# Performance work log

Hardware: AMD Instinct MI355X
Metric: run time of the kernel (lower is better)

## Reference

```python
import jax, jax.numpy as jnp
import numpy as np

VOCAB, EMBED, HIDDEN, NCLS = 50257, 64, 64, 5
B, S = 4096, 512
BN_EPS = 1e-5


def setup_inputs() -> dict:
    key = jax.random.key(0)
    ks = jax.random.split(key, 10)
    x = jax.random.randint(ks[0], (B, S), 0, VOCAB, dtype=jnp.int64 if jax.config.jax_enable_x64 else jnp.int32)
    emb = jax.random.normal(ks[1], (VOCAB, EMBED), dtype=jnp.float32)
    emb = emb.at[0].set(0.0)  # padding_idx=0
    s = 1.0 / np.sqrt(HIDDEN)
    W_ih = jax.random.uniform(ks[2], (HIDDEN, EMBED), minval=-s, maxval=s, dtype=jnp.float32)
    W_hh = jax.random.uniform(ks[3], (HIDDEN, HIDDEN), minval=-s, maxval=s, dtype=jnp.float32)
    b_ih = jax.random.uniform(ks[4], (HIDDEN,), minval=-s, maxval=s, dtype=jnp.float32)
    b_hh = jax.random.uniform(ks[5], (HIDDEN,), minval=-s, maxval=s, dtype=jnp.float32)
    gamma = jnp.ones((HIDDEN,), dtype=jnp.float32)
    beta = jnp.zeros((HIDDEN,), dtype=jnp.float32)
    sf = 1.0 / np.sqrt(HIDDEN)
    W_fc = jax.random.uniform(ks[6], (NCLS, HIDDEN), minval=-sf, maxval=sf, dtype=jnp.float32)
    b_fc = jax.random.uniform(ks[7], (NCLS,), minval=-sf, maxval=sf, dtype=jnp.float32)
    return {"x": x, "emb": emb, "W_ih": W_ih, "W_hh": W_hh, "b_ih": b_ih,
            "b_hh": b_hh, "gamma": gamma, "beta": beta, "W_fc": W_fc, "b_fc": b_fc}


def reference(x, emb, W_ih, W_hh, b_ih, b_hh, gamma, beta, W_fc, b_fc):
    # embedding gather: [B, S, E]
    xe = emb[x]
    # precompute input projection once: [B, S, H] -> scan over time as [S, B, H]
    xp = jnp.einsum('bse,he->bsh', xe, W_ih) + b_ih + b_hh
    xp_t = jnp.swapaxes(xp, 0, 1)

    def step(h, xt):
        h = jnp.tanh(xt + h @ W_hh.T)
        return h, None

    h0 = jnp.zeros((x.shape[0], HIDDEN), dtype=xp.dtype)
    h_n, _ = jax.lax.scan(step, h0, xp_t)

    # BatchNorm1d (training-mode math: batch stats, biased variance)
    mean = jnp.mean(h_n, axis=0)
    var = jnp.mean((h_n - mean) ** 2, axis=0)
    h_bn = (h_n - mean) * jax.lax.rsqrt(var + BN_EPS) * gamma + beta
    # dropout is identity in eval / deterministic reference
    logits = h_bn @ W_fc.T + b_fc  # [B, 5]
    return logits
```

## Files before the change

kernel.cpp:

```cpp
#include <hip/hip_runtime.h>

typedef unsigned short u16;
typedef __attribute__((ext_vector_type(8))) short bf16x8;
typedef __attribute__((ext_vector_type(4))) float f32x4;
typedef __attribute__((ext_vector_type(4))) u16 u16x4;

constexpr int BATCH  = 4096;
constexpr int SEQ    = 512;
constexpr int HID    = 64;
constexpr int EMB_N4 = 50257 * 64 / 4;

__device__ __forceinline__ float bf2f(u16 u) {
  union { unsigned int i; float f; } c; c.i = ((unsigned int)u) << 16; return c.f;
}
__device__ __forceinline__ u16 f2bf(float f) {
  union { float f; unsigned int i; } c; c.f = f;
  unsigned int u = c.i;
  u += 0x7fffu + ((u >> 16) & 1u);
  return (u16)(u >> 16);
}

#define MFMA16(a, b, c) __builtin_amdgcn_mfma_f32_16x16x32_bf16(a, b, c, 0, 0, 0)

__global__ __launch_bounds__(256) void prep_kernel(
    const float4* __restrict__ emb4, const float* __restrict__ Wih,
    const float* __restrict__ Whh, u16x4* __restrict__ emb_bf4,
    u16* __restrict__ wih_hi, u16* __restrict__ whh_hi, u16* __restrict__ whh_lo,
    float* __restrict__ bn_acc)
{
  int gid = blockIdx.x * 256 + threadIdx.x;
  if (gid < EMB_N4) {
    float4 v = emb4[gid];
    u16x4 o;
    o.x = f2bf(v.x); o.y = f2bf(v.y); o.z = f2bf(v.z); o.w = f2bf(v.w);
    emb_bf4[gid] = o;
  } else if (gid < EMB_N4 + 1024) {
    int i0 = (gid - EMB_N4) * 4;
    #pragma unroll
    for (int k = 0; k < 4; ++k) {
      int i = i0 + k;
      wih_hi[i] = f2bf(Wih[i]);
      float w = Whh[i];
      u16 hi = f2bf(w);
      whh_hi[i] = hi;
      whh_lo[i] = f2bf(w - bf2f(hi));
    }
  } else if (gid < EMB_N4 + 1024 + 128) {
    bn_acc[gid - (EMB_N4 + 1024)] = 0.f;
  }
}

__global__ __launch_bounds__(256, 1) void rnn_scan_kernel(
    const int* __restrict__ xx, const u16* __restrict__ emb_bf,
    const u16* __restrict__ wih_hi, const u16* __restrict__ whh_hi,
    const u16* __restrict__ whh_lo,
    const float* __restrict__ b_ih, const float* __restrict__ b_hh,
    float* __restrict__ hT , float* __restrict__ bn_acc)
{
  __shared__ u16 hbuf[2 * 2048];
  const int tid = threadIdx.x;
  const int w = tid >> 6;
  const int L = tid & 63;
  const int n = L & 15;
  const int q = L >> 4;
  const int R0 = blockIdx.x << 4;
  const int row  = R0 + n;
  const int feat = (w << 4) + n;

  ((int4*)hbuf)[tid] = int4{0, 0, 0, 0};

  bf16x8 Bih0 = *(const bf16x8*)(wih_hi + feat * 64 +      8 * q);
  bf16x8 Bih1 = *(const bf16x8*)(wih_hi + feat * 64 + 32 + 8 * q);
  bf16x8 Bh0  = *(const bf16x8*)(whh_hi + feat * 64 +      8 * q);
  bf16x8 Bh1  = *(const bf16x8*)(whh_hi + feat * 64 + 32 + 8 * q);
  bf16x8 Bl0  = *(const bf16x8*)(whh_lo + feat * 64 +      8 * q);
  bf16x8 Bl1  = *(const bf16x8*)(whh_lo + feat * 64 + 32 + 8 * q);
  const float bias = b_ih[feat] + b_hh[feat];

  const int r0off = n * 64 + (((0 + q) ^ (n & 7)) << 3);
  const int r1off = n * 64 + (((4 + q) ^ (n & 7)) << 3);
  const int cwbase = (w << 1) + (n >> 3);

  const int4* x4 = (const int4*)(xx + row * SEQ);
  int4 K1 = x4[1];

  bf16x8 e0[4], e1[4];
  {
    int4 K0 = x4[0];
    const int id0[4] = {K0.x, K0.y, K0.z, K0.w};
    #pragma unroll
    for (int u = 0; u < 4; ++u) {
      const u16* eb = emb_bf + (long)id0[u] * 64 + 8 * q;
      e0[u] = *(const bf16x8*)(eb);
      e1[u] = *(const bf16x8*)(eb + 32);
    }
  }

  __syncthreads();

  for (int t = 0; t < SEQ / 4; ++t) {
    int4 K2 = x4[(t + 2 < SEQ / 4) ? t + 2 : SEQ / 4 - 1];
    const int nid[4] = {K1.x, K1.y, K1.z, K1.w};
    const bool lastt = (t == SEQ / 4 - 1);

    #pragma unroll
    for (int u = 0; u < 4; ++u) {
      const int p = u & 1;
      const u16* hb = hbuf + p * 2048;
      bf16x8 ah0 = *(const bf16x8*)(hb + r0off);
      bf16x8 ah1 = *(const bf16x8*)(hb + r1off);
      bf16x8 al0 = *(const bf16x8*)(hb + 1024 + r0off);
      bf16x8 al1 = *(const bf16x8*)(hb + 1024 + r1off);

      f32x4 C1 = {bias, bias, bias, bias};
      C1 = MFMA16(e0[u], Bih0, C1);
      C1 = MFMA16(e1[u], Bih1, C1);

      {
        const u16* eb = emb_bf + (long)nid[u] * 64 + 8 * q;
        e0[u] = *(const bf16x8*)(eb);
        e1[u] = *(const bf16x8*)(eb + 32);
      }

      f32x4 Cx = {0.f, 0.f, 0.f, 0.f};
      f32x4 Cy = {0.f, 0.f, 0.f, 0.f};
      f32x4 Cz = {0.f, 0.f, 0.f, 0.f};
      Cx = MFMA16(ah0, Bh0, Cx);  Cx = MFMA16(al0, Bh0, Cx);
      Cy = MFMA16(ah1, Bh1, Cy);  Cy = MFMA16(al1, Bh1, Cy);
      Cz = MFMA16(ah0, Bl0, Cz);  Cz = MFMA16(ah1, Bl1, Cz);

      u16* wb = hbuf + (p ^ 1) * 2048;
      float th4[4];
      #pragma unroll
      for (int r = 0; r < 4; ++r) {
        float v = (C1[r] + Cx[r]) + (Cy[r] + Cz[r]);
        float ex = __builtin_amdgcn_exp2f(2.8853900817779268f * v);
        float th = fmaf(-2.0f, __builtin_amdgcn_rcpf(ex + 1.0f), 1.0f);
        th4[r] = th;
        const int mw = (q << 2) + r;
        const int off = mw * 64 + ((cwbase ^ (mw & 7)) << 3) + (n & 7);
        unsigned int tb = __float_as_uint(th);
        wb[off] = (u16)(tb >> 16);
        wb[1024 + off] = (u16)(__float_as_uint(th - __uint_as_float(tb & 0xffff0000u)) >> 16);
      }

      if (u == 3 && lastt) {
        float s1 = 0.f, s2 = 0.f;
        #pragma unroll
        for (int r = 0; r < 4; ++r) {
          hT[feat * BATCH + R0 + (q << 2) + r] = th4[r];
          s1 += th4[r];
          s2 = fmaf(th4[r], th4[r], s2);
        }
        s1 += __shfl_xor(s1, 16, 64);  s2 += __shfl_xor(s2, 16, 64);
        s1 += __shfl_xor(s1, 32, 64);  s2 += __shfl_xor(s2, 32, 64);
        if (q == 0) {
          atomicAdd(bn_acc + feat, s1);
          atomicAdd(bn_acc + 64 + feat, s2);
        }
      }

      asm volatile("s_waitcnt lgkmcnt(0)\n\ts_barrier" ::: "memory");
    }
    K1 = K2;
  }
}

__global__ __launch_bounds__(256) void head_kernel(
    const float* __restrict__ hT, const float* __restrict__ bn_acc,
    const float* __restrict__ gamma, const float* __restrict__ beta,
    const float* __restrict__ Wfc, const float* __restrict__ bfc,
    float* __restrict__ out)
{
  __shared__ float sc[64], sh[64];
  const int tid = threadIdx.x;
  if (tid < 64) {
    float mean = bn_acc[tid] * (1.0f / BATCH);
    float var  = bn_acc[64 + tid] * (1.0f / BATCH) - mean * mean;
    float inv  = rsqrtf(var + 1e-5f);
    float s    = gamma[tid] * inv;
    sc[tid] = s;
    sh[tid] = beta[tid] - mean * s;
  }
  __syncthreads();
  const int b = blockIdx.x * 256 + tid;
  float acc[5];
  #pragma unroll
  for (int c = 0; c < 5; ++c) acc[c] = bfc[c];
  for (int j = 0; j < HID; ++j) {
    float hv  = hT[j * BATCH + b];
    float hat = fmaf(hv, sc[j], sh[j]);
    #pragma unroll
    for (int c = 0; c < 5; ++c) acc[c] = fmaf(hat, Wfc[c * 64 + j], acc[c]);
  }
  #pragma unroll
  for (int c = 0; c < 5; ++c) out[b * 5 + c] = acc[c];
}

extern "C" void kernel_launch(void* const* d_in, const int* in_sizes, int n_in,
                              void* d_out, int out_size, void* d_ws, size_t ws_size,
                              hipStream_t stream)
{
  const int*   x     = (const int*)d_in[0];
  const float* emb   = (const float*)d_in[1];
  const float* W_ih  = (const float*)d_in[2];
  const float* W_hh  = (const float*)d_in[3];
  const float* b_ih  = (const float*)d_in[4];
  const float* b_hh  = (const float*)d_in[5];
  const float* gamma = (const float*)d_in[6];
  const float* beta  = (const float*)d_in[7];
  const float* W_fc  = (const float*)d_in[8];
  const float* b_fc  = (const float*)d_in[9];

  char* ws = (char*)d_ws;
  float* hT     = (float*)ws;
  float* bn_acc = (float*)(ws + 1048576);
  u16*   emb_bf = (u16*)(ws + 1049088);
  u16*   wih_hi = (u16*)(ws + 7481984);
  u16*   whh_hi = (u16*)(ws + 7490176);
  u16*   whh_lo = (u16*)(ws + 7498368);

  const int prep_items = EMB_N4 + 1024 + 128;
  prep_kernel<<<dim3((prep_items + 255) / 256), dim3(256), 0, stream>>>(
      (const float4*)emb, W_ih, W_hh, (u16x4*)emb_bf, wih_hi, whh_hi, whh_lo, bn_acc);
  rnn_scan_kernel<<<dim3(BATCH / 16), dim3(256), 0, stream>>>(
      x, emb_bf, wih_hi, whh_hi, whh_lo, b_ih, b_hh, hT, bn_acc);
  head_kernel<<<dim3(BATCH / 256), dim3(256), 0, stream>>>(
      hT, bn_acc, gamma, beta, W_fc, b_fc, (float*)d_out);
}
```

Baseline: 250.7 us.

## Stream embedding rows into an LDS ring via global_load_lds, pack hidden hi/lo

Instead of every wave loading embedding rows into registers, wave 0 issues asynchronous global-to-LDS DMA loads into an 8-slot shared ring several timesteps ahead, and all waves read the current slot from LDS. The hidden-state hi/lo bf16 halves are packed into one 32-bit word per element with a new swizzle, so each step needs one LDS store per value and the reads are unpacked with perm instructions. The intent is to hide embedding-gather latency and cut LDS store traffic on the serial recurrence. The cost is more LDS use, a vmcnt-based wait that only wave 0 performs, and index bookkeeping that is easy to get wrong.

Measured after the change: 315.1 us. 25.7% more time.

```diff
diff --git a/kernel.cpp b/kernel.cpp
--- a/kernel.cpp
+++ b/kernel.cpp
@@ -1,6 +1,7 @@
 #include <hip/hip_runtime.h>
 
 typedef unsigned short u16;
+typedef unsigned int u32;
 typedef __attribute__((ext_vector_type(8))) short bf16x8;
 typedef __attribute__((ext_vector_type(4))) float f32x4;
 typedef __attribute__((ext_vector_type(4))) u16 u16x4;
@@ -11,16 +12,35 @@
 constexpr int EMB_N4 = 50257 * 64 / 4;
 
 __device__ __forceinline__ float bf2f(u16 u) {
-  union { unsigned int i; float f; } c; c.i = ((unsigned int)u) << 16; return c.f;
+  union { u32 i; float f; } c; c.i = ((u32)u) << 16; return c.f;
 }
 __device__ __forceinline__ u16 f2bf(float f) {
-  union { float f; unsigned int i; } c; c.f = f;
-  unsigned int u = c.i;
+  union { float f; u32 i; } c; c.f = f;
+  u32 u = c.i;
   u += 0x7fffu + ((u >> 16) & 1u);
   return (u16)(u >> 16);
 }
 
 #define MFMA16(a, b, c) __builtin_amdgcn_mfma_f32_16x16x32_bf16(a, b, c, 0, 0, 0)
+
+__device__ __forceinline__ void glds16(const u16* g, u16* l) {
+  __builtin_amdgcn_global_load_lds(
+      (const __attribute__((address_space(1))) u32*)g,
+      (__attribute__((address_space(3))) u32*)l, 16, 0, 0);
+}
+
+__device__ __forceinline__ void unpack2(uint4 a, uint4 b, bf16x8& hi, bf16x8& lo) {
+  union { u32 u[4]; bf16x8 v; } H, L;
+  H.u[0] = __builtin_amdgcn_perm(a.y, a.x, 0x05040100u);
+  H.u[1] = __builtin_amdgcn_perm(a.w, a.z, 0x05040100u);
+  H.u[2] = __builtin_amdgcn_perm(b.y, b.x, 0x05040100u);
+  H.u[3] = __builtin_amdgcn_perm(b.w, b.z, 0x05040100u);
+  L.u[0] = __builtin_amdgcn_perm(a.y, a.x, 0x07060302u);
+  L.u[1] = __builtin_amdgcn_perm(a.w, a.z, 0x07060302u);
+  L.u[2] = __builtin_amdgcn_perm(b.y, b.x, 0x07060302u);
+  L.u[3] = __builtin_amdgcn_perm(b.w, b.z, 0x07060302u);
+  hi = H.v; lo = L.v;
+}
 
 __global__ __launch_bounds__(256) void prep_kernel(
     const float4* __restrict__ emb4, const float* __restrict__ Wih,
@@ -57,17 +77,17 @@
     const float* __restrict__ b_ih, const float* __restrict__ b_hh,
     float* __restrict__ hT , float* __restrict__ bn_acc)
 {
-  __shared__ u16 hbuf[2 * 2048];
+  __shared__ u32 hpk[2 * 1024];
+  __shared__ u16 ring[8 * 1024];
   const int tid = threadIdx.x;
   const int w = tid >> 6;
   const int L = tid & 63;
   const int n = L & 15;
   const int q = L >> 4;
   const int R0 = blockIdx.x << 4;
-  const int row  = R0 + n;
   const int feat = (w << 4) + n;
 
-  ((int4*)hbuf)[tid] = int4{0, 0, 0, 0};
+  ((int4*)hpk)[tid] = int4{0, 0, 0, 0};
 
   bf16x8 Bih0 = *(const bf16x8*)(wih_hi + feat * 64 +      8 * q);
   bf16x8 Bih1 = *(const bf16x8*)(wih_hi + feat * 64 + 32 + 8 * q);
@@ -77,50 +97,57 @@
   bf16x8 Bl1  = *(const bf16x8*)(whh_lo + feat * 64 + 32 + 8 * q);
   const float bias = b_ih[feat] + b_hh[feat];
 
-  const int r0off = n * 64 + (((0 + q) ^ (n & 7)) << 3);
-  const int r1off = n * 64 + (((4 + q) ^ (n & 7)) << 3);
-  const int cwbase = (w << 1) + (n >> 3);
-
-  const int4* x4 = (const int4*)(xx + row * SEQ);
-  int4 K1 = x4[1];
-
-  bf16x8 e0[4], e1[4];
-  {
+  const int sw   = ((n >> 2) & 1) << 4;
+  const int roff = n * 64 + ((8 * q) ^ sw);
+  const int wcol = feat ^ ((q & 1) << 4);
+  const int e0off = (q * 16 + n) * 8;
+
+  const int4* x4 = (const int4*)(xx + (R0 + n) * SEQ);
+  int4 JA = {0,0,0,0}, JB = {0,0,0,0};
+
+  if (w == 0) {
     int4 K0 = x4[0];
-    const int id0[4] = {K0.x, K0.y, K0.z, K0.w};
+    int4 K1 = x4[1];
+    const int pre[8] = {K0.x, K0.y, K0.z, K0.w, K1.x, K1.y, K1.z, 0};
+    #pragma unroll
+    for (int p = 0; p < 7; ++p) {
+      const u16* gp = emb_bf + (long)pre[p] * 64 + q * 8;
+      u16* lp = ring + p * 1024;
+      glds16(gp, lp);
+      glds16(gp + 32, lp + 512);
+    }
+    JA = K1;
+    JB = x4[2];
+  }
+
+  __syncthreads();
+
+  for (int t = 0; t < SEQ / 4; ++t) {
+    const int sbase = (t & 1) << 2;
+    int4 JC = {0,0,0,0};
+
     #pragma unroll
     for (int u = 0; u < 4; ++u) {
-      const u16* eb = emb_bf + (long)id0[u] * 64 + 8 * q;
-      e0[u] = *(const bf16x8*)(eb);
-      e1[u] = *(const bf16x8*)(eb + 32);
-    }
-  }
-
-  __syncthreads();
-
-  for (int t = 0; t < SEQ / 4; ++t) {
-    int4 K2 = x4[(t + 2 < SEQ / 4) ? t + 2 : SEQ / 4 - 1];
-    const int nid[4] = {K1.x, K1.y, K1.z, K1.w};
-    const bool lastt = (t == SEQ / 4 - 1);
-
-    #pragma unroll
-    for (int u = 0; u < 4; ++u) {
-      const int p = u & 1;
-      const u16* hb = hbuf + p * 2048;
-      bf16x8 ah0 = *(const bf16x8*)(hb + r0off);
-      bf16x8 ah1 = *(const bf16x8*)(hb + r1off);
-      bf16x8 al0 = *(const bf16x8*)(hb + 1024 + r0off);
-      bf16x8 al1 = *(const bf16x8*)(hb + 1024 + r1off);
+      const int cur = u & 1;
+      const int slot_rd  = sbase + u;
+      const int slot_dma = (sbase + u + 7) & 7;
+
+      const u16* rp = ring + slot_rd * 1024;
+      bf16x8 ae0 = *(const bf16x8*)(rp + e0off);
+      bf16x8 ae1 = *(const bf16x8*)(rp + 512 + e0off);
+
+      const u32* hb = hpk + cur * 1024;
+      uint4 vl0 = *(const uint4*)(hb + roff);
+      uint4 vl1 = *(const uint4*)(hb + roff + 4);
+      uint4 vh0 = *(const uint4*)(hb + roff + 32);
+      uint4 vh1 = *(const uint4*)(hb + roff + 36);
+      bf16x8 ah0, al0, ah1, al1;
+      unpack2(vl0, vl1, ah0, al0);
+      unpack2(vh0, vh1, ah1, al1);
 
       f32x4 C1 = {bias, bias, bias, bias};
-      C1 = MFMA16(e0[u], Bih0, C1);
-      C1 = MFMA16(e1[u], Bih1, C1);
-
-      {
-        const u16* eb = emb_bf + (long)nid[u] * 64 + 8 * q;
-        e0[u] = *(const bf16x8*)(eb);
-        e1[u] = *(const bf16x8*)(eb + 32);
-      }
+      C1 = MFMA16(ae0, Bih0, C1);
+      C1 = MFMA16(ae1, Bih1, C1);
 
       f32x4 Cx = {0.f, 0.f, 0.f, 0.f};
       f32x4 Cy = {0.f, 0.f, 0.f, 0.f};
@@ -129,7 +156,19 @@
       Cy = MFMA16(ah1, Bh1, Cy);  Cy = MFMA16(al1, Bh1, Cy);
       Cz = MFMA16(ah0, Bl0, Cz);  Cz = MFMA16(ah1, Bl1, Cz);
 
-      u16* wb = hbuf + (p ^ 1) * 2048;
+      if (w == 0) {
+        const int idxv = (u == 0) ? JA.w : (u == 1) ? JB.x : (u == 2) ? JB.y : JB.z;
+        const u16* gp = emb_bf + (long)idxv * 64 + q * 8;
+        u16* lp = ring + slot_dma * 1024;
+        glds16(gp, lp);
+        glds16(gp + 32, lp + 512);
+        if (u == 0) {
+          int tc = (t + 3 < SEQ / 4) ? t + 3 : SEQ / 4 - 1;
+          JC = x4[tc];
+        }
+      }
+
+      u32* wb = hpk + (cur ^ 1) * 1024;
       float th4[4];
       #pragma unroll
       for (int r = 0; r < 4; ++r) {
@@ -137,14 +176,13 @@
         float ex = __builtin_amdgcn_exp2f(2.8853900817779268f * v);
         float th = fmaf(-2.0f, __builtin_amdgcn_rcpf(ex + 1.0f), 1.0f);
         th4[r] = th;
-        const int mw = (q << 2) + r;
-        const int off = mw * 64 + ((cwbase ^ (mw & 7)) << 3) + (n & 7);
-        unsigned int tb = __float_as_uint(th);
-        wb[off] = (u16)(tb >> 16);
-        wb[1024 + off] = (u16)(__float_as_uint(th - __uint_as_float(tb & 0xffff0000u)) >> 16);
+        u32 tb = __float_as_uint(th);
+        u32 remb = __float_as_uint(th - __uint_as_float(tb & 0xffff0000u));
+        u32 packed = __builtin_amdgcn_perm(remb, tb, 0x07060302u);
+        wb[((q << 2) + r) * 64 + wcol] = packed;
       }
 
-      if (u == 3 && lastt) {
+      if (t == SEQ / 4 - 1 && u == 3) {
         float s1 = 0.f, s2 = 0.f;
         #pragma unroll
         for (int r = 0; r < 4; ++r) {
@@ -160,9 +198,12 @@
         }
       }
 
-      asm volatile("s_waitcnt lgkmcnt(0)\n\ts_barrier" ::: "memory");
+      if (w == 0)
+        asm volatile("s_waitcnt vmcnt(12) lgkmcnt(0)\n\ts_barrier" ::: "memory");
+      else
+        asm volatile("s_waitcnt lgkmcnt(0)\n\ts_barrier" ::: "memory");
     }
-    K1 = K2;
+    if (w == 0) { JA = JB; JB = JC; }
   }
 }
 
```

## Halve rows per RNN block to run two blocks per CU

Applied to the files above, without the earlier changes.

Each scan block now handles 8 batch rows instead of 16, so the grid doubles to 512 blocks. The launch bounds now allow two blocks per CU, which lets two independent recurrences interleave and hide MFMA, LDS and barrier latency in the serial time loop. The 16-row MFMA tile still runs in full, with the rows duplicated, so only half of the lanes write hidden state and contribute to the BN statistics. The cost is doubled MFMA work per useful row and higher register pressure, since the kernel must now fit two blocks per CU.

New measurement: 350.0 us. 39.6% more time.

```diff
diff --git a/kernel.cpp b/kernel.cpp
--- a/kernel.cpp
+++ b/kernel.cpp
@@ -1,6 +1,7 @@
 #include <hip/hip_runtime.h>
 
 typedef unsigned short u16;
+typedef unsigned int u32;
 typedef __attribute__((ext_vector_type(8))) short bf16x8;
 typedef __attribute__((ext_vector_type(4))) float f32x4;
 typedef __attribute__((ext_vector_type(4))) u16 u16x4;
@@ -8,14 +9,15 @@
 constexpr int BATCH  = 4096;
 constexpr int SEQ    = 512;
 constexpr int HID    = 64;
+constexpr int ROWS   = 8;
 constexpr int EMB_N4 = 50257 * 64 / 4;
 
 __device__ __forceinline__ float bf2f(u16 u) {
-  union { unsigned int i; float f; } c; c.i = ((unsigned int)u) << 16; return c.f;
+  union { u32 i; float f; } c; c.i = ((u32)u) << 16; return c.f;
 }
 __device__ __forceinline__ u16 f2bf(float f) {
-  union { float f; unsigned int i; } c; c.f = f;
-  unsigned int u = c.i;
+  union { float f; u32 i; } c; c.f = f;
+  u32 u = c.i;
   u += 0x7fffu + ((u >> 16) & 1u);
   return (u16)(u >> 16);
 }
@@ -50,7 +52,7 @@
   }
 }
 
-__global__ __launch_bounds__(256, 1) void rnn_scan_kernel(
+__global__ __launch_bounds__(256, 2) void rnn_scan_kernel(
     const int* __restrict__ xx, const u16* __restrict__ emb_bf,
     const u16* __restrict__ wih_hi, const u16* __restrict__ whh_hi,
     const u16* __restrict__ whh_lo,
@@ -63,11 +65,13 @@
   const int L = tid & 63;
   const int n = L & 15;
   const int q = L >> 4;
-  const int R0 = blockIdx.x << 4;
-  const int row  = R0 + n;
+  const int R0 = blockIdx.x << 3;
+  const int rm = n & 7;
+  const int row  = R0 + rm;
   const int feat = (w << 4) + n;
 
-  ((int4*)hbuf)[tid] = int4{0, 0, 0, 0};
+  ((int4*)hbuf)[tid]       = int4{0, 0, 0, 0};
+  ((int4*)hbuf)[tid + 256] = int4{0, 0, 0, 0};
 
   bf16x8 Bih0 = *(const bf16x8*)(wih_hi + feat * 64 +      8 * q);
   bf16x8 Bih1 = *(const bf16x8*)(wih_hi + feat * 64 + 32 + 8 * q);
@@ -77,8 +81,8 @@
   bf16x8 Bl1  = *(const bf16x8*)(whh_lo + feat * 64 + 32 + 8 * q);
   const float bias = b_ih[feat] + b_hh[feat];
 
-  const int r0off = n * 64 + (((0 + q) ^ (n & 7)) << 3);
-  const int r1off = n * 64 + (((4 + q) ^ (n & 7)) << 3);
+  const int r0off = rm * 64 + ((q ^ rm) << 3);
+  const int r1off = rm * 64 + (((4 + q) ^ rm) << 3);
   const int cwbase = (w << 1) + (n >> 3);
 
   const int4* x4 = (const int4*)(xx + row * SEQ);
@@ -137,23 +141,27 @@
         float ex = __builtin_amdgcn_exp2f(2.8853900817779268f * v);
         float th = fmaf(-2.0f, __builtin_amdgcn_rcpf(ex + 1.0f), 1.0f);
         th4[r] = th;
-        const int mw = (q << 2) + r;
-        const int off = mw * 64 + ((cwbase ^ (mw & 7)) << 3) + (n & 7);
-        unsigned int tb = __float_as_uint(th);
-        wb[off] = (u16)(tb >> 16);
-        wb[1024 + off] = (u16)(__float_as_uint(th - __uint_as_float(tb & 0xffff0000u)) >> 16);
+        if (q < 2) {
+          const int mw = (q << 2) + r;
+          const int off = mw * 64 + ((cwbase ^ (mw & 7)) << 3) + (n & 7);
+          u32 tb = __float_as_uint(th);
+          wb[off] = (u16)(tb >> 16);
+          wb[1024 + off] = (u16)(__float_as_uint(th - __uint_as_float(tb & 0xffff0000u)) >> 16);
+        }
       }
 
-      if (u == 3 && lastt) {
+      if (lastt && u == 3) {
         float s1 = 0.f, s2 = 0.f;
-        #pragma unroll
-        for (int r = 0; r < 4; ++r) {
-          hT[feat * BATCH + R0 + (q << 2) + r] = th4[r];
-          s1 += th4[r];
-          s2 = fmaf(th4[r], th4[r], s2);
+        if (q < 2) {
+          #pragma unroll
+          for (int r = 0; r < 4; ++r) {
+            hT[feat * BATCH + R0 + (q << 2) + r] = th4[r];
+            s1 += th4[r];
+            s2 = fmaf(th4[r], th4[r], s2);
+          }
         }
-        s1 += __shfl_xor(s1, 16, 64);  s2 += __shfl_xor(s2, 16, 64);
-        s1 += __shfl_xor(s1, 32, 64);  s2 += __shfl_xor(s2, 32, 64);
+        s1 += __shfl_xor(s1, 16, 64);
+        s2 += __shfl_xor(s2, 16, 64);
         if (q == 0) {
           atomicAdd(bn_acc + feat, s1);
           atomicAdd(bn_acc + 64 + feat, s2);
@@ -223,7 +231,7 @@
   const int prep_items = EMB_N4 + 1024 + 128;
   prep_kernel<<<dim3((prep_items + 255) / 256), dim3(256), 0, stream>>>(
       (const float4*)emb, W_ih, W_hh, (u16x4*)emb_bf, wih_hi, whh_hi, whh_lo, bn_acc);
-  rnn_scan_kernel<<<dim3(BATCH / 16), dim3(256), 0, stream>>>(
+  rnn_scan_kernel<<<dim3(BATCH / ROWS), dim3(256), 0, stream>>>(
       x, emb_bf, wih_hi, whh_hi, whh_lo, b_ih, b_hh, hT, bn_acc);
   head_kernel<<<dim3(BATCH / 256), dim3(256), 0, stream>>>(
       hT, bn_acc, gamma, beta, W_fc, b_fc, (float*)d_out);
```
